# Kernel optimization log

Hardware: AMD Instinct MI355X
Metric: run time of the kernel (lower is better)

## Reference

```python
import jax, jax.numpy as jnp
import numpy as np


def _cdist(a, b):
    # Euclidean distance between rows of a [M,D] and b [K,D] -> [M,K]
    a2 = jnp.sum(a * a, axis=-1)[:, None]
    b2 = jnp.sum(b * b, axis=-1)[None, :]
    d2 = a2 + b2 - 2.0 * (a @ b.T)
    return jnp.sqrt(jnp.maximum(d2, 1e-12))


def setup_inputs() -> dict:
    key = jax.random.key(0)
    k1, k2, k3 = jax.random.split(key, 3)
    L, N1, N2, P, D = 2, 8, 8, 1024, 768  # 2 output layers, 32x32 patches, ViT-B dim
    feats = jax.random.normal(k1, (L, N1, P, D), dtype=jnp.float32)
    nfeats = jax.random.normal(k2, (L, N2, P, D), dtype=jnp.float32)
    background_mask = jax.random.uniform(k3, (N1, P), dtype=jnp.float32)
    return {
        "feats": feats,
        "nfeats": nfeats,
        "background_mask": background_mask,
        "img_h": 512,
        "img_w": 512,
        "patch_size": 16,
    }


def reference(feats, nfeats, background_mask, img_h, img_w, patch_size):
    L, N1, P, D = feats.shape
    N2 = nfeats.shape[1]
    PH = img_h // patch_size
    PW = img_w // patch_size

    # L2-normalize patch features (as in Model.forward)
    f = feats / jnp.linalg.norm(feats, axis=-1, keepdims=True)
    nf = nfeats / jnp.linalg.norm(nfeats, axis=-1, keepdims=True)

    scores_list, pixel_list = [], []
    for l in range(L):  # small fixed number of output layers
        a = f[l].reshape(N1 * P, D)
        b = nf[l].reshape(N2 * P, D)
        # [N1,P,N2,P] -> [N1,N2,P,P], halved as in the original
        d = _cdist(a, b).reshape(N1, P, N2, P).transpose(0, 2, 1, 3) / 2.0
        sp = jnp.min(d, axis=-1)                       # [N1,N2,P] nearest normal patch
        sp = sp * background_mask[:, None, :]          # mask background patches
        sc = jnp.mean(jnp.max(sp, axis=-1), axis=-1)   # [N1] image score
        spatch = jnp.mean(sp, axis=1).reshape(N1, PH, PW)
        # bilinear, align_corners=False (half-pixel centers)
        spix = jax.image.resize(spatch, (N1, img_h, img_w), method="bilinear")
        scores_list.append(sc)
        pixel_list.append(spix)

    scores = jnp.mean(jnp.stack(scores_list, axis=0), axis=0)        # [N1]
    scores_pixel = jnp.mean(jnp.stack(pixel_list, axis=0), axis=0)   # [N1,H,W]
    return scores, scores_pixel
```

## Files before the change

### kernel.cpp

```cpp
#include <hip/hip_runtime.h>
#include <hip/hip_bf16.h>

using bf16 = __hip_bfloat16;
typedef __attribute__((ext_vector_type(8))) short short8;
typedef __attribute__((ext_vector_type(4))) float f32x4;

#define NLAY 2
#define NN1 8
#define NN2 8
#define PP 1024
#define DD 768
#define MROWS (NN1*PP)
#define BM 256
#define BN 256
#define BK 64
#define NKT (DD/BK)
#define NCT (MROWS/BN)

__global__ __launch_bounds__(256) void normalize_kernel(
    const float* __restrict__ in0, const float* __restrict__ in1,
    bf16* __restrict__ out0, bf16* __restrict__ out1) {
  int row  = blockIdx.x * 4 + (threadIdx.x >> 6);
  int lane = threadIdx.x & 63;
  const int half = NLAY * MROWS;
  const float* src;
  bf16* dst;
  if (row < half) { src = in0 + (size_t)row * DD;          dst = out0 + (size_t)row * DD; }
  else            { src = in1 + (size_t)(row - half) * DD; dst = out1 + (size_t)(row - half) * DD; }
  float4 v[3];
  float ss = 0.f;
#pragma unroll
  for (int i = 0; i < 3; i++) {
    v[i] = *reinterpret_cast<const float4*>(src + lane * 4 + i * 256);
    ss += v[i].x * v[i].x + v[i].y * v[i].y + v[i].z * v[i].z + v[i].w * v[i].w;
  }
#pragma unroll
  for (int off = 1; off < 64; off <<= 1) ss += __shfl_xor(ss, off);
  float rn = rsqrtf(ss);
#pragma unroll
  for (int i = 0; i < 3; i++) {
    bf16 tmp[4];
    tmp[0] = __float2bfloat16(v[i].x * rn);
    tmp[1] = __float2bfloat16(v[i].y * rn);
    tmp[2] = __float2bfloat16(v[i].z * rn);
    tmp[3] = __float2bfloat16(v[i].w * rn);
    *reinterpret_cast<uint2*>(dst + lane * 4 + i * 256) =
        *reinterpret_cast<const uint2*>(tmp);
  }
}


__device__ __forceinline__ short8 ld_frag(const bf16* h, int r, int slot) {
  return *reinterpret_cast<const short8*>(h + r * 64 + (((slot) ^ (r & 7)) << 3));
}

#define STAGE(Gbase, Lds) do {                                                  \
  _Pragma("unroll")                                                             \
  for (int i_ = 0; i_ < 2; i_++) {                                              \
    int u_ = i_ * 512 + t;                                                      \
    int r_ = u_ >> 3, s_ = u_ & 7;                                              \
    int sc_ = ((s_ ^ (r_ & 7)) << 3);                                           \
    __builtin_amdgcn_global_load_lds(                                           \
      (const __attribute__((address_space(1))) void*)((Gbase) + (size_t)r_ * DD + sc_), \
      (__attribute__((address_space(3))) void*)((Lds) + u_ * 8), 16, 0, 0);     \
  } } while (0)

#define VM2 asm volatile("s_waitcnt vmcnt(2)" ::: "memory")
#define VM0 asm volatile("s_waitcnt vmcnt(0)" ::: "memory")

#define LOAD_A(buf, qm)                                                         \
  _Pragma("unroll") for (int m_ = 0; m_ < 4; m_++)                              \
  _Pragma("unroll") for (int ks_ = 0; ks_ < 2; ks_++)                           \
    af_[m_][ks_] = ld_frag(&As[buf][qm][0], wr * 64 + m_ * 16 + rrow, ks_ * 4 + krow);

#define LOAD_B(buf)                                                             \
  _Pragma("unroll") for (int q_ = 0; q_ < 2; q_++)                              \
  _Pragma("unroll") for (int n_ = 0; n_ < 2; n_++)                              \
  _Pragma("unroll") for (int ks_ = 0; ks_ < 2; ks_++)                           \
    bf_[q_][n_][ks_] = ld_frag(&Bs[buf][q_][0], wc * 32 + n_ * 16 + rrow, ks_ * 4 + krow);

#define PHASEQ(buf, qm, LDB, STG, VMC) do {                                     \
  LOAD_A(buf, qm);                                                              \
  LDB;                                                                          \
  STG;                                                                          \
  __builtin_amdgcn_s_barrier();                                                 \
  asm volatile("s_waitcnt lgkmcnt(0)" ::: "memory");                            \
  __builtin_amdgcn_s_setprio(1);                                                \
  _Pragma("unroll") for (int q_ = 0; q_ < 2; q_++)                              \
  _Pragma("unroll") for (int n_ = 0; n_ < 2; n_++)                              \
  _Pragma("unroll") for (int m_ = 0; m_ < 4; m_++)                              \
  _Pragma("unroll") for (int ks_ = 0; ks_ < 2; ks_++)                           \
    acc[(qm) * 4 + m_][q_ * 2 + n_] = __builtin_amdgcn_mfma_f32_16x16x32_bf16(  \
        af_[m_][ks_], bf_[q_][n_][ks_], acc[(qm) * 4 + m_][q_ * 2 + n_], 0, 0, 0); \
  __builtin_amdgcn_s_setprio(0);                                                \
  VMC;                                                                          \
  __builtin_amdgcn_s_barrier();                                                 \
} while (0)

__global__ __launch_bounds__(512, 2) void gemm_max_kernel(
    const bf16* __restrict__ A, const bf16* __restrict__ Bm,
    float* __restrict__ partials) {
  __shared__ bf16 As[2][2][128 * 64];
  __shared__ bf16 Bs[2][2][128 * 64];
  __shared__ float red[4][256];

  const int id  = blockIdx.x;
  const int xcd = id & 7, p = id >> 3;
  const int l     = xcd >> 2;
  const int q     = p & 31, rnd = p >> 5;
  const int tiler = (xcd & 3) * 8 + (q & 7);
  const int tilec = rnd * 4 + (q >> 3);

  const bf16* Ab = A  + ((size_t)l * MROWS + (size_t)tiler * BM) * DD;
  const bf16* Bb = Bm + ((size_t)l * MROWS + (size_t)tilec * BN) * DD;

  const int t    = threadIdx.x;
  const int lane = t & 63;
  const int wave = t >> 6;
  const int wr   = wave >> 2;
  const int wc   = wave & 3;
  const int rrow = lane & 15;
  const int krow = lane >> 4;

  f32x4 acc[8][4];
#pragma unroll
  for (int m = 0; m < 8; m++)
#pragma unroll
    for (int n = 0; n < 4; n++) acc[m][n] = (f32x4){0.f, 0.f, 0.f, 0.f};

  STAGE(Ab,                      &As[0][0][0]);
  STAGE(Ab + (size_t)128 * DD,   &As[0][1][0]);
  STAGE(Bb,                      &Bs[0][0][0]);
  STAGE(Bb + (size_t)128 * DD,   &Bs[0][1][0]);
  STAGE(Ab + BK,                 &As[1][0][0]);
  VM2;
  __builtin_amdgcn_s_barrier();

  for (int i = 0; i < NKT / 2; i++) {
    const int O = 2 * i + 1, E2 = 2 * i + 2, O2 = 2 * i + 3;
    short8 af_[4][2], bf_[2][2][2];
    PHASEQ(0, 0, LOAD_B(0),
      { STAGE(Ab + (size_t)128 * DD + (size_t)O * BK, &As[1][1][0]);
        STAGE(Bb + (size_t)O * BK,                    &Bs[1][0][0]);
        STAGE(Bb + (size_t)128 * DD + (size_t)O * BK, &Bs[1][1][0]); }, (void)0);
    PHASEQ(0, 1, (void)0,
      if (E2 < NKT) STAGE(Ab + (size_t)E2 * BK, &As[0][0][0]),
      if (E2 < NKT) { VM2; } else { VM0; });
    PHASEQ(1, 0, LOAD_B(1),
      if (E2 < NKT) { STAGE(Ab + (size_t)128 * DD + (size_t)E2 * BK, &As[0][1][0]);
                      STAGE(Bb + (size_t)E2 * BK,                    &Bs[0][0][0]);
                      STAGE(Bb + (size_t)128 * DD + (size_t)E2 * BK, &Bs[0][1][0]); }, (void)0);
    PHASEQ(1, 1, (void)0,
      if (O2 < NKT) STAGE(Ab + (size_t)O2 * BK, &As[1][0][0]),
      if (O2 < NKT) { VM2; });
  }

#pragma unroll
  for (int m = 0; m < 8; m++) {
#pragma unroll
    for (int j = 0; j < 4; j++) {
      float v = acc[m][0][j];
      v = fmaxf(v, acc[m][1][j]);
      v = fmaxf(v, acc[m][2][j]);
      v = fmaxf(v, acc[m][3][j]);
#pragma unroll
      for (int off = 1; off < 16; off <<= 1) v = fmaxf(v, __shfl_xor(v, off));
      if (rrow == 0) {
        int row = (m >> 2) * 128 + wr * 64 + (m & 3) * 16 + krow * 4 + j;
        red[wc][row] = v;
      }
    }
  }
  __syncthreads();
  if (t < 256) {
    float v = fmaxf(fmaxf(red[0][t], red[1][t]), fmaxf(red[2][t], red[3][t]));
    partials[((size_t)l * MROWS + (size_t)tiler * BM + t) * NCT + tilec] = v;
  }
}

__global__ __launch_bounds__(1024) void reduce_kernel(
    const float* __restrict__ partials, const float* __restrict__ mask,
    float* __restrict__ scores, float* __restrict__ spatch) {
  const int n1 = blockIdx.x;
  const int p  = threadIdx.x;
  const int row = n1 * PP + p;
  const float mk = mask[row];

  float sp[16];
  float ssum = 0.f;
#pragma unroll
  for (int l = 0; l < NLAY; l++) {
    const float* pr = partials + ((size_t)l * MROWS + row) * NCT;
#pragma unroll
    for (int n2 = 0; n2 < NN2; n2++) {
      float md = pr[n2 * 4];
#pragma unroll
      for (int tt = 1; tt < 4; tt++) md = fmaxf(md, pr[n2 * 4 + tt]);
      float d2 = fmaxf(2.f - 2.f * md, 1e-12f);
      float s  = 0.5f * sqrtf(d2) * mk;
      sp[l * 8 + n2] = s;
      ssum += s;
    }
  }
  spatch[row] = ssum * (1.f / 16.f);

  __shared__ float wred[16][16];
  __shared__ float sres[16];
  const int lane = p & 63;
  const int wave = p >> 6;
#pragma unroll
  for (int v = 0; v < 16; v++) {
    float x = sp[v];
#pragma unroll
    for (int off = 1; off < 64; off <<= 1) x = fmaxf(x, __shfl_xor(x, off));
    if (lane == 0) wred[wave][v] = x;
  }
  __syncthreads();
  if (p < 16) {
    float x = wred[0][p];
#pragma unroll
    for (int w = 1; w < 16; w++) x = fmaxf(x, wred[w][p]);
    sres[p] = x;
  }
  __syncthreads();
  if (p == 0) {
    float s = 0.f;
#pragma unroll
    for (int v = 0; v < 16; v++) s += sres[v];
    scores[n1] = s * (1.f / 16.f);
  }
}

__global__ __launch_bounds__(256) void upsample_kernel(
    const float* __restrict__ spatch, float* __restrict__ out) {
  int idx = blockIdx.x * 256 + threadIdx.x;
  if (idx >= NN1 * 512 * 512) return;
  int x = idx & 511;
  int y = (idx >> 9) & 511;
  int n = idx >> 18;
  float sx = (x + 0.5f) * 0.0625f - 0.5f;
  float sy = (y + 0.5f) * 0.0625f - 0.5f;
  int x0 = (int)floorf(sx); float wx = sx - (float)x0;
  int y0 = (int)floorf(sy); float wy = sy - (float)y0;
  int x1 = min(x0 + 1, 31); x0 = max(x0, 0);
  int y1 = min(y0 + 1, 31); y0 = max(y0, 0);
  const float* s = spatch + n * PP;
  float v00 = s[y0 * 32 + x0], v01 = s[y0 * 32 + x1];
  float v10 = s[y1 * 32 + x0], v11 = s[y1 * 32 + x1];
  float v = (1.f - wy) * ((1.f - wx) * v00 + wx * v01) +
            wy * ((1.f - wx) * v10 + wx * v11);
  out[idx] = v;
}

extern "C" void kernel_launch(void* const* d_in, const int* in_sizes, int n_in,
                              void* d_out, int out_size, void* d_ws, size_t ws_size,
                              hipStream_t stream) {
  const float* feats  = (const float*)d_in[0];
  const float* nfeats = (const float*)d_in[1];
  const float* mask   = (const float*)d_in[2];
  float* out = (float*)d_out;

  bf16* Abf = (bf16*)d_ws;
  bf16* Bbf = Abf + (size_t)NLAY * MROWS * DD;
  float* partials = (float*)(Bbf + (size_t)NLAY * MROWS * DD);
  float* spatch   = partials + (size_t)NLAY * MROWS * NCT;

  normalize_kernel<<<(2 * NLAY * MROWS) / 4, 256, 0, stream>>>(feats, nfeats, Abf, Bbf);

  gemm_max_kernel<<<NCT * (MROWS / BM) * NLAY, 512, 0, stream>>>(Abf, Bbf, partials);

  reduce_kernel<<<NN1, 1024, 0, stream>>>(partials, mask, out, spatch);

  upsample_kernel<<<(NN1 * 512 * 512) / 256, 256, 0, stream>>>(spatch, out + 8);
}
```

Before: 360.3 us.

## Fuse reduce and upsample kernels; trim barriers in GEMM phase loop

The separate upsample kernel is folded into the reduce kernel. The patch scores stay in shared memory, and each of the 8 blocks writes its image's 512x512 map with float4 stores, which removes one launch and the spatch round-trip through global memory. The GEMM phase macro now uses a single barrier at the start of each phase instead of two, and the explicit lgkmcnt wait is dropped in favour of compiler-inserted waits, to cut synchronization stalls. The risk is that only 8 CUs now write the whole 8 MB pixel output, which may be bandwidth-limited per CU.

```diff
diff --git a/kernel.cpp b/kernel.cpp
--- a/kernel.cpp
+++ b/kernel.cpp
@@ -80,11 +80,10 @@
     bf_[q_][n_][ks_] = ld_frag(&Bs[buf][q_][0], wc * 32 + n_ * 16 + rrow, ks_ * 4 + krow);
 
 #define PHASEQ(buf, qm, LDB, STG, VMC) do {                                     \
+  __builtin_amdgcn_s_barrier();                                                 \
   LOAD_A(buf, qm);                                                              \
   LDB;                                                                          \
   STG;                                                                          \
-  __builtin_amdgcn_s_barrier();                                                 \
-  asm volatile("s_waitcnt lgkmcnt(0)" ::: "memory");                            \
   __builtin_amdgcn_s_setprio(1);                                                \
   _Pragma("unroll") for (int q_ = 0; q_ < 2; q_++)                              \
   _Pragma("unroll") for (int n_ = 0; n_ < 2; n_++)                              \
@@ -94,7 +93,6 @@
         af_[m_][ks_], bf_[q_][n_][ks_], acc[(qm) * 4 + m_][q_ * 2 + n_], 0, 0, 0); \
   __builtin_amdgcn_s_setprio(0);                                                \
   VMC;                                                                          \
-  __builtin_amdgcn_s_barrier();                                                 \
 } while (0)
 
 __global__ __launch_bounds__(512, 2) void gemm_max_kernel(
@@ -134,7 +132,6 @@
   STAGE(Bb + (size_t)128 * DD,   &Bs[0][1][0]);
   STAGE(Ab + BK,                 &As[1][0][0]);
   VM2;
-  __builtin_amdgcn_s_barrier();
 
   for (int i = 0; i < NKT / 2; i++) {
     const int O = 2 * i + 1, E2 = 2 * i + 2, O2 = 2 * i + 3;
@@ -178,14 +175,16 @@
   }
 }
 
-__global__ __launch_bounds__(1024) void reduce_kernel(
+__global__ __launch_bounds__(1024) void reduce_upsample_kernel(
     const float* __restrict__ partials, const float* __restrict__ mask,
-    float* __restrict__ scores, float* __restrict__ spatch) {
+    float* __restrict__ scores, float* __restrict__ outpix) {
   const int n1 = blockIdx.x;
   const int p  = threadIdx.x;
   const int row = n1 * PP + p;
   const float mk = mask[row];
 
+  __shared__ float sp_s[PP];
+
   float sp[16];
   float ssum = 0.f;
 #pragma unroll
@@ -193,16 +192,15 @@
     const float* pr = partials + ((size_t)l * MROWS + row) * NCT;
 #pragma unroll
     for (int n2 = 0; n2 < NN2; n2++) {
-      float md = pr[n2 * 4];
-#pragma unroll
-      for (int tt = 1; tt < 4; tt++) md = fmaxf(md, pr[n2 * 4 + tt]);
+      float4 v4 = *reinterpret_cast<const float4*>(pr + n2 * 4);
+      float md = fmaxf(fmaxf(v4.x, v4.y), fmaxf(v4.z, v4.w));
       float d2 = fmaxf(2.f - 2.f * md, 1e-12f);
       float s  = 0.5f * sqrtf(d2) * mk;
       sp[l * 8 + n2] = s;
       ssum += s;
     }
   }
-  spatch[row] = ssum * (1.f / 16.f);
+  sp_s[p] = ssum * (1.f / 16.f);
 
   __shared__ float wred[16][16];
   __shared__ float sres[16];
@@ -229,27 +227,31 @@
     for (int v = 0; v < 16; v++) s += sres[v];
     scores[n1] = s * (1.f / 16.f);
   }
-}
-
-__global__ __launch_bounds__(256) void upsample_kernel(
-    const float* __restrict__ spatch, float* __restrict__ out) {
-  int idx = blockIdx.x * 256 + threadIdx.x;
-  if (idx >= NN1 * 512 * 512) return;
-  int x = idx & 511;
-  int y = (idx >> 9) & 511;
-  int n = idx >> 18;
-  float sx = (x + 0.5f) * 0.0625f - 0.5f;
-  float sy = (y + 0.5f) * 0.0625f - 0.5f;
-  int x0 = (int)floorf(sx); float wx = sx - (float)x0;
-  int y0 = (int)floorf(sy); float wy = sy - (float)y0;
-  int x1 = min(x0 + 1, 31); x0 = max(x0, 0);
-  int y1 = min(y0 + 1, 31); y0 = max(y0, 0);
-  const float* s = spatch + n * PP;
-  float v00 = s[y0 * 32 + x0], v01 = s[y0 * 32 + x1];
-  float v10 = s[y1 * 32 + x0], v11 = s[y1 * 32 + x1];
-  float v = (1.f - wy) * ((1.f - wx) * v00 + wx * v01) +
-            wy * ((1.f - wx) * v10 + wx * v11);
-  out[idx] = v;
+
+  float* dst = outpix + (size_t)n1 * 512 * 512;
+#pragma unroll 1
+  for (int it = 0; it < 64; it++) {
+    int idx4 = it * 1024 + p;
+    int x0i  = (idx4 & 127) * 4;
+    int y    = idx4 >> 7;
+    float sy = (y + 0.5f) * 0.0625f - 0.5f;
+    int yy0 = (int)floorf(sy); float wy = sy - (float)yy0;
+    int yy1 = min(yy0 + 1, 31); yy0 = max(yy0, 0);
+    const float* r0 = sp_s + yy0 * 32;
+    const float* r1 = sp_s + yy1 * 32;
+    float4 o;
+#pragma unroll
+    for (int k = 0; k < 4; k++) {
+      int x = x0i + k;
+      float sx = (x + 0.5f) * 0.0625f - 0.5f;
+      int xx0 = (int)floorf(sx); float wx = sx - (float)xx0;
+      int xx1 = min(xx0 + 1, 31); xx0 = max(xx0, 0);
+      float v0 = (1.f - wx) * r0[xx0] + wx * r0[xx1];
+      float v1 = (1.f - wx) * r1[xx0] + wx * r1[xx1];
+      ((float*)&o)[k] = (1.f - wy) * v0 + wy * v1;
+    }
+    *reinterpret_cast<float4*>(dst + idx4 * 4) = o;
+  }
 }
 
 extern "C" void kernel_launch(void* const* d_in, const int* in_sizes, int n_in,
@@ -263,13 +265,10 @@
   bf16* Abf = (bf16*)d_ws;
   bf16* Bbf = Abf + (size_t)NLAY * MROWS * DD;
   float* partials = (float*)(Bbf + (size_t)NLAY * MROWS * DD);
-  float* spatch   = partials + (size_t)NLAY * MROWS * NCT;
 
   normalize_kernel<<<(2 * NLAY * MROWS) / 4, 256, 0, stream>>>(feats, nfeats, Abf, Bbf);
 
   gemm_max_kernel<<<NCT * (MROWS / BM) * NLAY, 512, 0, stream>>>(Abf, Bbf, partials);
 
-  reduce_kernel<<<NN1, 1024, 0, stream>>>(partials, mask, out, spatch);
-
-  upsample_kernel<<<(NN1 * 512 * 512) / 256, 256, 0, stream>>>(spatch, out + 8);
-}
+  reduce_upsample_kernel<<<NN1, 1024, 0, stream>>>(partials, mask, out, out + 8);
+}
```

New measurement: 407.3 us. 1.13x slower.

## Split GEMM main loop into eight finer phases with deeper prefetch and transpose partials

Applied to the files above, without the earlier changes.

The GEMM main loop now runs eight smaller phases per pair of K tiles instead of four. Each phase issues a single staged global-to-LDS load, so loads are spread evenly and more of them stay in flight (vmcnt 6 instead of 2, with seven stages in the prologue). A sched_barrier keeps the MFMA block from being mixed with the LDS reads. The partials buffer is transposed to [layer][column tile][row], which makes the epilogue writes and the reduce kernel reads coalesced. The cost is twice as many block barriers per K step.

```diff
diff --git a/kernel.cpp b/kernel.cpp
--- a/kernel.cpp
+++ b/kernel.cpp
@@ -65,33 +65,31 @@
       (__attribute__((address_space(3))) void*)((Lds) + u_ * 8), 16, 0, 0);     \
   } } while (0)
 
-#define VM2 asm volatile("s_waitcnt vmcnt(2)" ::: "memory")
+#define VM6 asm volatile("s_waitcnt vmcnt(6)" ::: "memory")
 #define VM0 asm volatile("s_waitcnt vmcnt(0)" ::: "memory")
 
-#define LOAD_A(buf, qm)                                                         \
+#define LOAD_A(buf, mh)                                                         \
   _Pragma("unroll") for (int m_ = 0; m_ < 4; m_++)                              \
   _Pragma("unroll") for (int ks_ = 0; ks_ < 2; ks_++)                           \
-    af_[m_][ks_] = ld_frag(&As[buf][qm][0], wr * 64 + m_ * 16 + rrow, ks_ * 4 + krow);
-
-#define LOAD_B(buf)                                                             \
-  _Pragma("unroll") for (int q_ = 0; q_ < 2; q_++)                              \
+    af_[m_][ks_] = ld_frag(&As[buf][mh][0], wr * 64 + m_ * 16 + rrow, ks_ * 4 + krow);
+
+#define LOAD_BH(buf, h)                                                         \
   _Pragma("unroll") for (int n_ = 0; n_ < 2; n_++)                              \
   _Pragma("unroll") for (int ks_ = 0; ks_ < 2; ks_++)                           \
-    bf_[q_][n_][ks_] = ld_frag(&Bs[buf][q_][0], wc * 32 + n_ * 16 + rrow, ks_ * 4 + krow);
-
-#define PHASEQ(buf, qm, LDB, STG, VMC) do {                                     \
-  LOAD_A(buf, qm);                                                              \
-  LDB;                                                                          \
+    bf_[h][n_][ks_] = ld_frag(&Bs[buf][h][0], wc * 32 + n_ * 16 + rrow, ks_ * 4 + krow);
+
+#define PH(mh, bh, RDS, STG, VMC) do {                                          \
+  RDS;                                                                          \
   STG;                                                                          \
   __builtin_amdgcn_s_barrier();                                                 \
   asm volatile("s_waitcnt lgkmcnt(0)" ::: "memory");                            \
+  __builtin_amdgcn_sched_barrier(0);                                            \
   __builtin_amdgcn_s_setprio(1);                                                \
-  _Pragma("unroll") for (int q_ = 0; q_ < 2; q_++)                              \
   _Pragma("unroll") for (int n_ = 0; n_ < 2; n_++)                              \
   _Pragma("unroll") for (int m_ = 0; m_ < 4; m_++)                              \
   _Pragma("unroll") for (int ks_ = 0; ks_ < 2; ks_++)                           \
-    acc[(qm) * 4 + m_][q_ * 2 + n_] = __builtin_amdgcn_mfma_f32_16x16x32_bf16(  \
-        af_[m_][ks_], bf_[q_][n_][ks_], acc[(qm) * 4 + m_][q_ * 2 + n_], 0, 0, 0); \
+    acc[(mh) * 4 + m_][(bh) * 2 + n_] = __builtin_amdgcn_mfma_f32_16x16x32_bf16( \
+        af_[m_][ks_], bf_[bh][n_][ks_], acc[(mh) * 4 + m_][(bh) * 2 + n_], 0, 0, 0); \
   __builtin_amdgcn_s_setprio(0);                                                \
   VMC;                                                                          \
   __builtin_amdgcn_s_barrier();                                                 \
@@ -128,31 +126,37 @@
 #pragma unroll
     for (int n = 0; n < 4; n++) acc[m][n] = (f32x4){0.f, 0.f, 0.f, 0.f};
 
-  STAGE(Ab,                      &As[0][0][0]);
-  STAGE(Ab + (size_t)128 * DD,   &As[0][1][0]);
-  STAGE(Bb,                      &Bs[0][0][0]);
-  STAGE(Bb + (size_t)128 * DD,   &Bs[0][1][0]);
-  STAGE(Ab + BK,                 &As[1][0][0]);
-  VM2;
+  STAGE(Ab,                           &As[0][0][0]);
+  STAGE(Bb,                           &Bs[0][0][0]);
+  STAGE(Ab + (size_t)128 * DD,        &As[0][1][0]);
+  STAGE(Bb + (size_t)128 * DD,        &Bs[0][1][0]);
+  STAGE(Ab + BK,                      &As[1][0][0]);
+  STAGE(Bb + BK,                      &Bs[1][0][0]);
+  STAGE(Ab + (size_t)128 * DD + BK,   &As[1][1][0]);
+  VM6;
   __builtin_amdgcn_s_barrier();
 
   for (int i = 0; i < NKT / 2; i++) {
     const int O = 2 * i + 1, E2 = 2 * i + 2, O2 = 2 * i + 3;
     short8 af_[4][2], bf_[2][2][2];
-    PHASEQ(0, 0, LOAD_B(0),
-      { STAGE(Ab + (size_t)128 * DD + (size_t)O * BK, &As[1][1][0]);
-        STAGE(Bb + (size_t)O * BK,                    &Bs[1][0][0]);
-        STAGE(Bb + (size_t)128 * DD + (size_t)O * BK, &Bs[1][1][0]); }, (void)0);
-    PHASEQ(0, 1, (void)0,
-      if (E2 < NKT) STAGE(Ab + (size_t)E2 * BK, &As[0][0][0]),
-      if (E2 < NKT) { VM2; } else { VM0; });
-    PHASEQ(1, 0, LOAD_B(1),
-      if (E2 < NKT) { STAGE(Ab + (size_t)128 * DD + (size_t)E2 * BK, &As[0][1][0]);
-                      STAGE(Bb + (size_t)E2 * BK,                    &Bs[0][0][0]);
-                      STAGE(Bb + (size_t)128 * DD + (size_t)E2 * BK, &Bs[0][1][0]); }, (void)0);
-    PHASEQ(1, 1, (void)0,
-      if (O2 < NKT) STAGE(Ab + (size_t)O2 * BK, &As[1][0][0]),
-      if (O2 < NKT) { VM2; });
+    PH(0, 0, { LOAD_A(0, 0); LOAD_BH(0, 0); },
+       STAGE(Bb + (size_t)128 * DD + (size_t)O * BK, &Bs[1][1][0]), (void)0);
+    PH(0, 1, LOAD_BH(0, 1),
+       if (E2 < NKT) STAGE(Ab + (size_t)E2 * BK, &As[0][0][0]), (void)0);
+    PH(1, 0, LOAD_A(0, 1),
+       if (E2 < NKT) STAGE(Bb + (size_t)E2 * BK, &Bs[0][0][0]), (void)0);
+    PH(1, 1, (void)0,
+       if (E2 < NKT) STAGE(Ab + (size_t)128 * DD + (size_t)E2 * BK, &As[0][1][0]),
+       if (E2 < NKT) { VM6; } else { VM0; });
+    PH(0, 0, { LOAD_A(1, 0); LOAD_BH(1, 0); },
+       if (E2 < NKT) STAGE(Bb + (size_t)128 * DD + (size_t)E2 * BK, &Bs[0][1][0]), (void)0);
+    PH(0, 1, LOAD_BH(1, 1),
+       if (O2 < NKT) STAGE(Ab + (size_t)O2 * BK, &As[1][0][0]), (void)0);
+    PH(1, 0, LOAD_A(1, 1),
+       if (O2 < NKT) STAGE(Bb + (size_t)O2 * BK, &Bs[1][0][0]), (void)0);
+    PH(1, 1, (void)0,
+       if (O2 < NKT) STAGE(Ab + (size_t)128 * DD + (size_t)O2 * BK, &As[1][1][0]),
+       if (O2 < NKT) { VM6; });
   }
 
 #pragma unroll
@@ -174,7 +178,7 @@
   __syncthreads();
   if (t < 256) {
     float v = fmaxf(fmaxf(red[0][t], red[1][t]), fmaxf(red[2][t], red[3][t]));
-    partials[((size_t)l * MROWS + (size_t)tiler * BM + t) * NCT + tilec] = v;
+    partials[((size_t)l * NCT + tilec) * MROWS + (size_t)tiler * BM + t] = v;
   }
 }
 
@@ -190,12 +194,12 @@
   float ssum = 0.f;
 #pragma unroll
   for (int l = 0; l < NLAY; l++) {
-    const float* pr = partials + ((size_t)l * MROWS + row) * NCT;
 #pragma unroll
     for (int n2 = 0; n2 < NN2; n2++) {
-      float md = pr[n2 * 4];
-#pragma unroll
-      for (int tt = 1; tt < 4; tt++) md = fmaxf(md, pr[n2 * 4 + tt]);
+      const float* pr = partials + ((size_t)l * NCT + n2 * 4) * MROWS + row;
+      float md = pr[0];
+#pragma unroll
+      for (int tt = 1; tt < 4; tt++) md = fmaxf(md, pr[(size_t)tt * MROWS]);
       float d2 = fmaxf(2.f - 2.f * md, 1e-12f);
       float s  = 0.5f * sqrtf(d2) * mk;
       sp[l * 8 + n2] = s;
@@ -263,7 +267,7 @@
   bf16* Abf = (bf16*)d_ws;
   bf16* Bbf = Abf + (size_t)NLAY * MROWS * DD;
   float* partials = (float*)(Bbf + (size_t)NLAY * MROWS * DD);
-  float* spatch   = partials + (size_t)NLAY * MROWS * NCT;
+  float* spatch   = partials + (size_t)NLAY * NCT * MROWS;
 
   normalize_kernel<<<(2 * NLAY * MROWS) / 4, 256, 0, stream>>>(feats, nfeats, Abf, Bbf);
 
```

Result: no change. 355.7 us (-1.3%).
